# Optimization experiments

Hardware: AMD Instinct MI355X
Metric: run time of the kernel (lower is better)

Reference implementation:

```python
import jax, jax.numpy as jnp
import numpy as np

TAU = 0.07
EPS = 1e-6  # torch CosineSimilarity eps


def setup_inputs() -> dict:
    key = jax.random.key(0)
    k1, k2, k3 = jax.random.split(key, 3)
    n, d, n_classes = 8192, 256, 1024
    imitation_embeds = jax.random.normal(k1, (n, d), dtype=jnp.float32)
    recording_embeds = jax.random.normal(k2, (n, d), dtype=jnp.float32)
    labels = jax.random.randint(k3, (n,), 0, n_classes, dtype=jnp.int64)
    return {
        "imitation_embeds": imitation_embeds,
        "recording_embeds": recording_embeds,
        "labels": labels,
    }


def reference(imitation_embeds, recording_embeds, labels):
    n = imitation_embeds.shape[0]
    # cosine similarity with per-vector norm clamp (torch semantics)
    im_n = imitation_embeds / jnp.maximum(
        jnp.linalg.norm(imitation_embeds, axis=1, keepdims=True), EPS)
    rec_n = recording_embeds / jnp.maximum(
        jnp.linalg.norm(recording_embeds, axis=1, keepdims=True), EPS)
    i2r = jnp.einsum("nd,md->nm", im_n, rec_n) / TAU  # [n, n]

    same = labels[:, None] == labels[None, :]          # [n, n] bool
    eye = jnp.eye(n, dtype=bool)
    # original: mask = ~(same ^ diag_embed(diag(same))); diag(same) is all True
    # -> keep the diagonal (positive) and all different-label negatives
    mask = ~(same ^ eye)

    # per-row masked log-softmax evaluated at the diagonal entry:
    # log_softmax(row[mask])[pos_of_diag] = i2r[i,i] - logsumexp(row over mask)
    lse = jax.nn.logsumexp(jnp.where(mask, i2r, -jnp.inf), axis=1)  # [n]
    loss = -jnp.mean(jnp.diagonal(i2r) - lse)
    return loss
```

## Files before the change

kernel.cpp:

```cpp
#include <hip/hip_runtime.h>

#define N 8192
#define D 256
#define INV_TAU 14.285714285714286f
#define EPSN 1e-6f

#define RT 128
#define CT 64
#define CSPLIT 16
#define CPB (N / CSPLIT)
#define NTILES (CPB / CT)
#define LDSS 264

typedef unsigned int u32x4 __attribute__((ext_vector_type(4)));
typedef __bf16 bf16x8 __attribute__((ext_vector_type(8)));
typedef float f32x4 __attribute__((ext_vector_type(4)));

__device__ inline unsigned short f2bf(float x) {
    unsigned int u = __builtin_bit_cast(unsigned int, x);
    u += 0x7fffu + ((u >> 16) & 1u);
    return (unsigned short)(u >> 16);
}

__global__ void ntx_prep(const float* __restrict__ im, const float* __restrict__ rec,
                         unsigned short* __restrict__ A, unsigned short* __restrict__ Bm,
                         float* __restrict__ diag, float* __restrict__ rowsum) {
    const int wave = threadIdx.x >> 6;
    const int lane = threadIdx.x & 63;
    const int row  = blockIdx.x * 4 + wave;

    const float4 a = ((const float4*)(im  + (size_t)row * D))[lane];
    const float4 b = ((const float4*)(rec + (size_t)row * D))[lane];

    float ssa = a.x*a.x + a.y*a.y + a.z*a.z + a.w*a.w;
    float ssb = b.x*b.x + b.y*b.y + b.z*b.z + b.w*b.w;
    float dt  = a.x*b.x + a.y*b.y + a.z*b.z + a.w*b.w;
    #pragma unroll
    for (int o = 32; o; o >>= 1) {
        ssa += __shfl_xor(ssa, o);
        ssb += __shfl_xor(ssb, o);
        dt  += __shfl_xor(dt , o);
    }
    const float ra = 1.0f / fmaxf(sqrtf(ssa), EPSN);
    const float rb = 1.0f / fmaxf(sqrtf(ssb), EPSN);

    ushort4 pa, pb;
    pa.x = f2bf(a.x*ra); pa.y = f2bf(a.y*ra); pa.z = f2bf(a.z*ra); pa.w = f2bf(a.w*ra);
    pb.x = f2bf(b.x*rb); pb.y = f2bf(b.y*rb); pb.z = f2bf(b.z*rb); pb.w = f2bf(b.w*rb);
    *(ushort4*)(A  + (size_t)row * D + lane * 4) = pa;
    *(ushort4*)(Bm + (size_t)row * D + lane * 4) = pb;

    if (lane == 0) {
        diag[row]   = dt * ra * rb * INV_TAU;
        rowsum[row] = 0.0f;
    }
}

__global__ __launch_bounds__(256, 2)
void ntx_lse(const unsigned short* __restrict__ A, const unsigned short* __restrict__ Bm,
             const int* __restrict__ labels, float* __restrict__ rowsum) {
    __shared__ __align__(16) unsigned short Bs[CT][LDSS];

    const int wave = threadIdx.x >> 6;
    const int lane = threadIdx.x & 63;
    const int g    = lane >> 4;
    const int n16  = lane & 15;

    const int rowblk = blockIdx.x & (N / RT - 1);
    const int colblk = blockIdx.x >> 6;
    const int row0 = rowblk * RT + wave * 32;
    const int col0 = colblk * CPB;

    bf16x8 afrag[2][8];
    #pragma unroll
    for (int rs = 0; rs < 2; ++rs) {
        const int r = row0 + rs * 16 + n16;
        #pragma unroll
        for (int k = 0; k < 8; ++k)
            afrag[rs][k] = __builtin_bit_cast(
                bf16x8, *(const u32x4*)(A + (size_t)r * D + k * 32 + g * 8));
    }

    int rlab[2][4];
    #pragma unroll
    for (int rs = 0; rs < 2; ++rs)
        #pragma unroll
        for (int q = 0; q < 4; ++q)
            rlab[rs][q] = labels[row0 + rs * 16 + g * 4 + q];

    float acc[2][4] = {{0.f,0.f,0.f,0.f},{0.f,0.f,0.f,0.f}};

    const int c32 = threadIdx.x & 31;
    const int rr  = threadIdx.x >> 5;

    for (int t = 0; t < NTILES; ++t) {
        const int colt = col0 + t * CT;
        #pragma unroll
        for (int p = 0; p < 8; ++p) {
            const int br = p * 8 + rr;
            u32x4 v = *(const u32x4*)(Bm + (size_t)(colt + br) * D + c32 * 8);
            *(u32x4*)(&Bs[br][c32 * 8]) = v;
        }
        __syncthreads();

        #pragma unroll
        for (int cs = 0; cs < 4; ++cs) {
            const int bc = cs * 16 + n16;
            bf16x8 bfrag[8];
            #pragma unroll
            for (int k = 0; k < 8; ++k)
                bfrag[k] = __builtin_bit_cast(
                    bf16x8, *(const u32x4*)(&Bs[bc][k * 32 + g * 8]));

            const int col  = colt + cs * 16 + n16;
            const int clab = labels[col];

            #pragma unroll
            for (int rs = 0; rs < 2; ++rs) {
                f32x4 c = {0.f, 0.f, 0.f, 0.f};
                #pragma unroll
                for (int k = 0; k < 8; ++k)
                    c = __builtin_amdgcn_mfma_f32_16x16x32_bf16(
                            afrag[rs][k], bfrag[k], c, 0, 0, 0);
                #pragma unroll
                for (int q = 0; q < 4; ++q) {
                    const int r = row0 + rs * 16 + g * 4 + q;
                    const float e = __expf(c[q] * INV_TAU);
                    const bool drop = (rlab[rs][q] == clab) && (r != col);
                    acc[rs][q] += drop ? 0.0f : e;
                }
            }
        }
        __syncthreads();
    }

    #pragma unroll
    for (int rs = 0; rs < 2; ++rs)
        #pragma unroll
        for (int q = 0; q < 4; ++q) {
            float v = acc[rs][q];
            v += __shfl_xor(v, 1);
            v += __shfl_xor(v, 2);
            v += __shfl_xor(v, 4);
            v += __shfl_xor(v, 8);
            if (n16 == 0)
                atomicAdd(&rowsum[row0 + rs * 16 + g * 4 + q], v);
        }
}

__global__ void ntx_finish(const float* __restrict__ diag,
                           const float* __restrict__ rowsum,
                           float* __restrict__ out) {
    __shared__ float red[256];
    float s = 0.f;
    for (int i = threadIdx.x; i < N; i += 256)
        s += logf(rowsum[i]) - diag[i];
    red[threadIdx.x] = s;
    __syncthreads();
    #pragma unroll
    for (int o = 128; o; o >>= 1) {
        if (threadIdx.x < o) red[threadIdx.x] += red[threadIdx.x + o];
        __syncthreads();
    }
    if (threadIdx.x == 0) out[0] = red[0] / (float)N;
}

extern "C" void kernel_launch(void* const* d_in, const int* in_sizes, int n_in,
                              void* d_out, int out_size, void* d_ws, size_t ws_size,
                              hipStream_t stream) {
    const float* im     = (const float*)d_in[0];
    const float* rec    = (const float*)d_in[1];
    const int*   labels = (const int*)d_in[2];
    float* out = (float*)d_out;

    unsigned short* A  = (unsigned short*)d_ws;
    unsigned short* Bm = A + (size_t)N * D;
    float* diag   = (float*)(Bm + (size_t)N * D);
    float* rowsum = diag + N;

    ntx_prep<<<N / 4, 256, 0, stream>>>(im, rec, A, Bm, diag, rowsum);
    ntx_lse<<<(N / RT) * CSPLIT, 256, 0, stream>>>(A, Bm, labels, rowsum);
    ntx_finish<<<1, 256, 0, stream>>>(diag, rowsum, out);
}
```

Baseline: 124.3 us.

## Remove label mask from hot loop via per-class correction, enlarge row tile

The main similarity/exp loop now sums exp over all columns with no label checks. A new correction kernel subtracts same-label, off-diagonal terms using per-class member lists built with atomics during prep. It also doubles the rows per block (RT 256, four 16-row MFMA subtiles per wave), loads B tiles directly into LDS with global_load_lds using an XOR-swizzled layout, and switches to exp2 with a pre-scaled constant. In exchange it adds a memset and an extra kernel launch, risks cancellation from subtracting large terms, and caps class membership at 48 entries, which is wrong if any class is larger.

```diff
diff --git a/kernel.cpp b/kernel.cpp
--- a/kernel.cpp
+++ b/kernel.cpp
@@ -3,14 +3,15 @@
 #define N 8192
 #define D 256
 #define INV_TAU 14.285714285714286f
+#define SCALE2 20.60992915555662f
 #define EPSN 1e-6f
-
-#define RT 128
+#define MAXM 48
+
+#define RT 256
 #define CT 64
 #define CSPLIT 16
 #define CPB (N / CSPLIT)
 #define NTILES (CPB / CT)
-#define LDSS 264
 
 typedef unsigned int u32x4 __attribute__((ext_vector_type(4)));
 typedef __bf16 bf16x8 __attribute__((ext_vector_type(8)));
@@ -21,10 +22,23 @@
     u += 0x7fffu + ((u >> 16) & 1u);
     return (unsigned short)(u >> 16);
 }
+__device__ inline float b2f(unsigned short u) {
+    unsigned int x = (unsigned int)u << 16;
+    return __builtin_bit_cast(float, x);
+}
+__device__ inline float fexp2(float x) {
+#if __has_builtin(__builtin_amdgcn_exp2f)
+    return __builtin_amdgcn_exp2f(x);
+#else
+    return __expf(x * 0.6931471805599453f);
+#endif
+}
 
 __global__ void ntx_prep(const float* __restrict__ im, const float* __restrict__ rec,
+                         const int* __restrict__ labels,
                          unsigned short* __restrict__ A, unsigned short* __restrict__ Bm,
-                         float* __restrict__ diag, float* __restrict__ rowsum) {
+                         float* __restrict__ diag, float* __restrict__ rowsum,
+                         int* __restrict__ cnt, unsigned short* __restrict__ members) {
     const int wave = threadIdx.x >> 6;
     const int lane = threadIdx.x & 63;
     const int row  = blockIdx.x * 4 + wave;
@@ -47,19 +61,25 @@
     ushort4 pa, pb;
     pa.x = f2bf(a.x*ra); pa.y = f2bf(a.y*ra); pa.z = f2bf(a.z*ra); pa.w = f2bf(a.w*ra);
     pb.x = f2bf(b.x*rb); pb.y = f2bf(b.y*rb); pb.z = f2bf(b.z*rb); pb.w = f2bf(b.w*rb);
-    *(ushort4*)(A  + (size_t)row * D + lane * 4) = pa;
-    *(ushort4*)(Bm + (size_t)row * D + lane * 4) = pb;
+
+    *(ushort4*)(A + (size_t)row * D + lane * 4) = pa;
+    const int chunk = lane >> 1;
+    const int sw = chunk ^ (row & 7);
+    *(ushort4*)(Bm + (size_t)row * D + sw * 8 + (lane & 1) * 4) = pb;
 
     if (lane == 0) {
         diag[row]   = dt * ra * rb * INV_TAU;
         rowsum[row] = 0.0f;
+        const int lab = labels[row];
+        const int u = atomicAdd(&cnt[lab], 1);
+        if (u < MAXM) members[lab * MAXM + u] = (unsigned short)row;
     }
 }
 
 __global__ __launch_bounds__(256, 2)
 void ntx_lse(const unsigned short* __restrict__ A, const unsigned short* __restrict__ Bm,
-             const int* __restrict__ labels, float* __restrict__ rowsum) {
-    __shared__ __align__(16) unsigned short Bs[CT][LDSS];
+             float* __restrict__ rowsum) {
+    __shared__ __align__(16) unsigned short Bs[CT][D];
 
     const int wave = threadIdx.x >> 6;
     const int lane = threadIdx.x & 63;
@@ -67,13 +87,13 @@
     const int n16  = lane & 15;
 
     const int rowblk = blockIdx.x & (N / RT - 1);
-    const int colblk = blockIdx.x >> 6;
-    const int row0 = rowblk * RT + wave * 32;
+    const int colblk = blockIdx.x >> 5;
+    const int row0 = rowblk * RT + wave * 64;
     const int col0 = colblk * CPB;
 
-    bf16x8 afrag[2][8];
-    #pragma unroll
-    for (int rs = 0; rs < 2; ++rs) {
+    bf16x8 afrag[4][8];
+    #pragma unroll
+    for (int rs = 0; rs < 4; ++rs) {
         const int r = row0 + rs * 16 + n16;
         #pragma unroll
         for (int k = 0; k < 8; ++k)
@@ -81,25 +101,22 @@
                 bf16x8, *(const u32x4*)(A + (size_t)r * D + k * 32 + g * 8));
     }
 
-    int rlab[2][4];
-    #pragma unroll
-    for (int rs = 0; rs < 2; ++rs)
-        #pragma unroll
-        for (int q = 0; q < 4; ++q)
-            rlab[rs][q] = labels[row0 + rs * 16 + g * 4 + q];
-
-    float acc[2][4] = {{0.f,0.f,0.f,0.f},{0.f,0.f,0.f,0.f}};
-
-    const int c32 = threadIdx.x & 31;
-    const int rr  = threadIdx.x >> 5;
+    float acc[4][4];
+    #pragma unroll
+    for (int rs = 0; rs < 4; ++rs)
+        #pragma unroll
+        for (int q = 0; q < 4; ++q) acc[rs][q] = 0.f;
 
     for (int t = 0; t < NTILES; ++t) {
-        const int colt = col0 + t * CT;
-        #pragma unroll
-        for (int p = 0; p < 8; ++p) {
-            const int br = p * 8 + rr;
-            u32x4 v = *(const u32x4*)(Bm + (size_t)(colt + br) * D + c32 * 8);
-            *(u32x4*)(&Bs[br][c32 * 8]) = v;
+        const char* gsrc = (const char*)(Bm + (size_t)(col0 + t * CT) * D);
+        char* lbase = (char*)&Bs[0][0];
+        #pragma unroll
+        for (int i = 0; i < 8; ++i) {
+            const int off = (i * 4 + wave) * 1024;
+            __builtin_amdgcn_global_load_lds(
+                (const __attribute__((address_space(1))) void*)(gsrc + off + lane * 16),
+                (__attribute__((address_space(3))) void*)(lbase + off),
+                16, 0, 0);
         }
         __syncthreads();
 
@@ -110,32 +127,25 @@
             #pragma unroll
             for (int k = 0; k < 8; ++k)
                 bfrag[k] = __builtin_bit_cast(
-                    bf16x8, *(const u32x4*)(&Bs[bc][k * 32 + g * 8]));
-
-            const int col  = colt + cs * 16 + n16;
-            const int clab = labels[col];
+                    bf16x8, *(const u32x4*)(&Bs[bc][((k * 4 + g) ^ (bc & 7)) * 8]));
 
             #pragma unroll
-            for (int rs = 0; rs < 2; ++rs) {
+            for (int rs = 0; rs < 4; ++rs) {
                 f32x4 c = {0.f, 0.f, 0.f, 0.f};
                 #pragma unroll
                 for (int k = 0; k < 8; ++k)
                     c = __builtin_amdgcn_mfma_f32_16x16x32_bf16(
                             afrag[rs][k], bfrag[k], c, 0, 0, 0);
                 #pragma unroll
-                for (int q = 0; q < 4; ++q) {
-                    const int r = row0 + rs * 16 + g * 4 + q;
-                    const float e = __expf(c[q] * INV_TAU);
-                    const bool drop = (rlab[rs][q] == clab) && (r != col);
-                    acc[rs][q] += drop ? 0.0f : e;
-                }
+                for (int q = 0; q < 4; ++q)
+                    acc[rs][q] += fexp2(c[q] * SCALE2);
             }
         }
         __syncthreads();
     }
 
     #pragma unroll
-    for (int rs = 0; rs < 2; ++rs)
+    for (int rs = 0; rs < 4; ++rs)
         #pragma unroll
         for (int q = 0; q < 4; ++q) {
             float v = acc[rs][q];
@@ -146,6 +156,37 @@
             if (n16 == 0)
                 atomicAdd(&rowsum[row0 + rs * 16 + g * 4 + q], v);
         }
+}
+
+__global__ void ntx_correct(const unsigned short* __restrict__ A,
+                            const unsigned short* __restrict__ Bm,
+                            const int* __restrict__ labels, const int* __restrict__ cnt,
+                            const unsigned short* __restrict__ members,
+                            float* __restrict__ rowsum) {
+    const int wave = threadIdx.x >> 6;
+    const int lane = threadIdx.x & 63;
+    const int W = blockIdx.x * 4 + wave;
+    const int chunk = lane >> 1;
+
+    for (int rr = 0; rr < 4; ++rr) {
+        const int r = W * 4 + rr;
+        const int lab = labels[r];
+        const int m = min(cnt[lab], MAXM);
+        const ushort4 av = *(const ushort4*)(A + (size_t)r * D + lane * 4);
+        const float a0 = b2f(av.x), a1 = b2f(av.y), a2 = b2f(av.z), a3 = b2f(av.w);
+        float sum = 0.f;
+        for (int t = 0; t < m; ++t) {
+            const int j = members[lab * MAXM + t];
+            if (j == r) continue;
+            const int sw = chunk ^ (j & 7);
+            const ushort4 bv = *(const ushort4*)(Bm + (size_t)j * D + sw * 8 + (lane & 1) * 4);
+            float d = a0 * b2f(bv.x) + a1 * b2f(bv.y) + a2 * b2f(bv.z) + a3 * b2f(bv.w);
+            #pragma unroll
+            for (int o = 32; o; o >>= 1) d += __shfl_xor(d, o);
+            sum += fexp2(d * SCALE2);
+        }
+        if (lane == 0) rowsum[r] -= sum;
+    }
 }
 
 __global__ void ntx_finish(const float* __restrict__ diag,
@@ -177,8 +218,12 @@
     unsigned short* Bm = A + (size_t)N * D;
     float* diag   = (float*)(Bm + (size_t)N * D);
     float* rowsum = diag + N;
-
-    ntx_prep<<<N / 4, 256, 0, stream>>>(im, rec, A, Bm, diag, rowsum);
-    ntx_lse<<<(N / RT) * CSPLIT, 256, 0, stream>>>(A, Bm, labels, rowsum);
+    int* cnt      = (int*)(rowsum + N);
+    unsigned short* members = (unsigned short*)(cnt + 1024);
+
+    hipMemsetAsync(cnt, 0, 1024 * sizeof(int), stream);
+    ntx_prep<<<N / 4, 256, 0, stream>>>(im, rec, labels, A, Bm, diag, rowsum, cnt, members);
+    ntx_lse<<<(N / RT) * CSPLIT, 256, 0, stream>>>(A, Bm, rowsum);
+    ntx_correct<<<N / 16, 256, 0, stream>>>(A, Bm, labels, cnt, members, rowsum);
     ntx_finish<<<1, 256, 0, stream>>>(diag, rowsum, out);
 }
```

Result: slower. 149.7 us (+20.5%).
